# Optimization experiments

Measured on AMD Instinct MI355X. Metric: run time of the kernel, lower is better.

## Reference

```python
import jax, jax.numpy as jnp
import numpy as np

BS, L, D, H, BLOCKS = 2, 8192, 1024, 16, 16
BC = L // BLOCKS          # block_ctx = 512
HD = D // H               # head dim = 64
SCALE2 = 1.0 / float(np.sqrt(HD))  # (scale*scale) with scale = HD**-0.25


def setup_inputs() -> dict:
    key = jax.random.key(0)
    k0, k1, k2 = jax.random.split(key, 3)
    return {
        "x": jax.random.normal(k0, (BS, L, D), jnp.float32),
        "w_attn": jax.random.normal(k1, (D, 3 * D), jnp.float32) * 0.02,
        "b_attn": jnp.zeros((3 * D,), jnp.float32),
        "w_proj": jax.random.normal(k2, (D, D), jnp.float32) * 0.02,
        "b_proj": jnp.zeros((D,), jnp.float32),
    }


def _block_attn(q, k, v):
    # q, k, v: [BS, L, D]; block-local causal attention (attn_func=1, eval path)
    nb = BS * BLOCKS
    def heads(x):
        # [BS, L, D] -> [nb, BC, D] -> [nb, H, BC, HD]
        return x.reshape(nb, BC, H, HD).transpose(0, 2, 1, 3)
    qh, kh, vh = heads(q), heads(k), heads(v)
    w = jnp.einsum('bhqd,bhkd->bhqk', qh, kh) * SCALE2          # [nb, H, BC, BC]
    w = w.astype(jnp.float32)
    mask = jnp.tril(jnp.ones((BC, BC), jnp.float32))
    w = w * mask + (-1e9) * (1.0 - mask)
    w = jax.nn.softmax(w, axis=-1)
    a = jnp.einsum('bhqk,bhkd->bhqd', w, vh)                    # [nb, H, BC, HD]
    return a.transpose(0, 2, 1, 3).reshape(BS, L, D)


def reference(x, w_attn, b_attn, w_proj, b_proj):
    qkv = x @ w_attn + b_attn                                   # Conv1D c_attn
    q, k, v = jnp.split(qkv, 3, axis=-1)
    a = _block_attn(q, k, v)
    return a @ w_proj + b_proj                                  # Conv1D c_proj
```

## Files before the change

### kernel.cpp

```cpp
#include <hip/hip_runtime.h>
#include <stdint.h>


typedef __bf16 bf16x8 __attribute__((ext_vector_type(8)));
typedef short short8 __attribute__((ext_vector_type(8)));
typedef float f32x4 __attribute__((ext_vector_type(4)));
typedef unsigned short ushort4v __attribute__((ext_vector_type(4)));
typedef unsigned short ushort8v __attribute__((ext_vector_type(8)));

#define GLOAD_LDS16(g, l)                                                      \
  __builtin_amdgcn_global_load_lds(                                            \
      (const __attribute__((address_space(1))) void*)(g),                      \
      (__attribute__((address_space(3))) void*)(l), 16, 0, 0)

static __device__ __forceinline__ f32x4 mfma16(short8 a, short8 b, f32x4 c) {
  return __builtin_amdgcn_mfma_f32_16x16x32_bf16(
      __builtin_bit_cast(bf16x8, a), __builtin_bit_cast(bf16x8, b), c, 0, 0, 0);
}

static __device__ __forceinline__ unsigned short f2bf(float f) {
  unsigned u = __builtin_bit_cast(unsigned, f);
  u += 0x7FFFu + ((u >> 16) & 1u);
  return (unsigned short)(u >> 16);
}

__global__ __launch_bounds__(256) void convert_bf16(
    const float* __restrict__ in, unsigned short* __restrict__ out, int n8) {
  for (int i = blockIdx.x * 256 + threadIdx.x; i < n8; i += gridDim.x * 256) {
    f32x4 lo = *(const f32x4*)(in + (size_t)i * 8);
    f32x4 hi = *(const f32x4*)(in + (size_t)i * 8 + 4);
    ushort8v v;
    v[0] = f2bf(lo[0]); v[1] = f2bf(lo[1]); v[2] = f2bf(lo[2]); v[3] = f2bf(lo[3]);
    v[4] = f2bf(hi[0]); v[5] = f2bf(hi[1]); v[6] = f2bf(hi[2]); v[7] = f2bf(hi[3]);
    *(ushort8v*)(out + (size_t)i * 8) = v;
  }
}

__global__ __launch_bounds__(256) void transposeW(
    const float* __restrict__ in, unsigned short* __restrict__ out,
    int K, int N) {
  __shared__ float tile[64][68];
  int tn = blockIdx.x * 64, tk = blockIdx.y * 64;
  int tid = threadIdx.x;
#pragma unroll
  for (int i = 0; i < 4; ++i) {
    int ch = i * 256 + tid;
    int r = ch >> 4, c4 = (ch & 15) << 2;
    f32x4 v = *(const f32x4*)(in + (size_t)(tk + r) * N + tn + c4);
    tile[r][c4] = v[0]; tile[r][c4 + 1] = v[1];
    tile[r][c4 + 2] = v[2]; tile[r][c4 + 3] = v[3];
  }
  __syncthreads();
#pragma unroll
  for (int i = 0; i < 4; ++i) {
    int ch = i * 256 + tid;
    int r = ch >> 4, c4 = (ch & 15) << 2;
    ushort4v v;
    v[0] = f2bf(tile[c4][r]);     v[1] = f2bf(tile[c4 + 1][r]);
    v[2] = f2bf(tile[c4 + 2][r]); v[3] = f2bf(tile[c4 + 3][r]);
    *(ushort4v*)(out + (size_t)(tn + r) * K + tk + c4) = v;
  }
}

template <bool C_F32>
__global__ __launch_bounds__(512, 2) void gemm256(
    const unsigned short* __restrict__ A, int lda,
    const unsigned short* __restrict__ Bt, int ldb,
    const float* __restrict__ bias,
    void* __restrict__ Cptr, int ldc,
    int Ntiles, int K) {
  __shared__ unsigned short sA[2][256 * 64];
  __shared__ unsigned short sB[2][256 * 64];
  int bid = blockIdx.x;
  int nwg = gridDim.x;
  int swz = (bid & 7) * (nwg >> 3) + (bid >> 3);
  int bm = swz / Ntiles, bn = swz % Ntiles;
  int tid = threadIdx.x;
  int lane = tid & 63, wave = tid >> 6;
  int wr = wave >> 2, wc = wave & 3;
  int g = lane >> 4, cx = lane & 15;

  const unsigned short* srcA[4];
  const unsigned short* srcB[4];
  int dstoff[4];
#pragma unroll
  for (int i = 0; i < 4; ++i) {
    int c = i * 512 + tid;
    int r = c >> 3, pc = c & 7;
    int cc = pc ^ (r & 7);
    srcA[i] = A + (size_t)(bm * 256 + r) * lda + cc * 8;
    srcB[i] = Bt + (size_t)(bn * 256 + r) * ldb + cc * 8;
    dstoff[i] = (i * 512 + wave * 64) * 8;
  }

  f32x4 zero4 = {0.f, 0.f, 0.f, 0.f};
  f32x4 acc[8][4];
#pragma unroll
  for (int a = 0; a < 8; ++a)
#pragma unroll
    for (int b = 0; b < 4; ++b) acc[a][b] = zero4;

  int NT = K >> 6;

#pragma unroll
  for (int i = 0; i < 4; ++i) {
    GLOAD_LDS16(srcA[i], sA[0] + dstoff[i]);
    GLOAD_LDS16(srcB[i], sB[0] + dstoff[i]);
  }

  for (int t = 0; t < NT; ++t) {
    int p = t & 1;
    asm volatile("s_waitcnt vmcnt(0)" ::: "memory");
    __builtin_amdgcn_sched_barrier(0);
    __builtin_amdgcn_s_barrier();
    __builtin_amdgcn_sched_barrier(0);

    const char* bA = (const char*)sA[p];
    const char* bB = (const char*)sB[p];
    bool pre = (t + 1 < NT);
    int kt = (t + 1) * 64;
    short8 bfr[4][2];

#pragma unroll
    for (int q = 0; q < 4; ++q) {
      if (q == 0) {
#pragma unroll
        for (int ni = 0; ni < 4; ++ni)
#pragma unroll
          for (int ks = 0; ks < 2; ++ks) {
            int row = wc * 64 + ni * 16 + cx;
            unsigned off = (unsigned)(row * 128 + ks * 64 + g * 16) ^
                           ((unsigned)(row & 7) << 4);
            bfr[ni][ks] = *(const short8*)(bB + off);
          }
      }
      short8 af[2][2];
#pragma unroll
      for (int mm = 0; mm < 2; ++mm)
#pragma unroll
        for (int ks = 0; ks < 2; ++ks) {
          int row = wr * 128 + (q * 2 + mm) * 16 + cx;
          unsigned off = (unsigned)(row * 128 + ks * 64 + g * 16) ^
                         ((unsigned)(row & 7) << 4);
          af[mm][ks] = *(const short8*)(bA + off);
        }
      if (pre) {
        GLOAD_LDS16(srcA[q] + kt, sA[p ^ 1] + dstoff[q]);
        GLOAD_LDS16(srcB[q] + kt, sB[p ^ 1] + dstoff[q]);
      }
      if (q == 0) asm volatile("s_waitcnt lgkmcnt(8)" ::: "memory");
      __builtin_amdgcn_sched_barrier(0);
      __builtin_amdgcn_s_barrier();
      asm volatile("s_waitcnt lgkmcnt(0)" ::: "memory");
      __builtin_amdgcn_sched_barrier(0);
      __builtin_amdgcn_s_setprio(1);
#pragma unroll
      for (int mm = 0; mm < 2; ++mm)
#pragma unroll
        for (int ni = 0; ni < 4; ++ni)
#pragma unroll
          for (int ks = 0; ks < 2; ++ks)
            acc[q * 2 + mm][ni] = mfma16(af[mm][ks], bfr[ni][ks],
                                         acc[q * 2 + mm][ni]);
      __builtin_amdgcn_s_setprio(0);
      __builtin_amdgcn_sched_barrier(0);
      __builtin_amdgcn_s_barrier();
      __builtin_amdgcn_sched_barrier(0);
    }
  }

  float bv[4];
#pragma unroll
  for (int ni = 0; ni < 4; ++ni)
    bv[ni] = bias[bn * 256 + wc * 64 + ni * 16 + cx];

#pragma unroll
  for (int mi = 0; mi < 8; ++mi)
#pragma unroll
    for (int ni = 0; ni < 4; ++ni) {
      int col = bn * 256 + wc * 64 + ni * 16 + cx;
#pragma unroll
      for (int ri = 0; ri < 4; ++ri) {
        int row = bm * 256 + wr * 128 + mi * 16 + g * 4 + ri;
        float v = acc[mi][ni][ri] + bv[ni];
        if (C_F32)
          ((float*)Cptr)[(size_t)row * ldc + col] = v;
        else
          ((unsigned short*)Cptr)[(size_t)row * ldc + col] = f2bf(v);
      }
    }
}

__global__ __launch_bounds__(256) void attn_block(unsigned short* __restrict__ qkv) {
  const int LDQ = 3072;
  int bid = blockIdx.x;
  int pair = bid & 1;
  int nbh = bid >> 1;
  int nb = nbh >> 4, h = nbh & 15;
  int rowblk = nb << 9;
  int tid = threadIdx.x, lane = tid & 63, wave = tid >> 6;
  int g = lane >> 4, cx = lane & 15;

  __shared__ unsigned short sK[64 * 64];
  __shared__ unsigned short sVT[64 * 64];
  __shared__ unsigned short sP[4][32 * 64];
  unsigned short* myP = sP[wave];

  const unsigned short* srcK[2];
  const unsigned short* srcV[2];
  unsigned short* dstK[2];
  int kr_[2], d8_[2];
#pragma unroll
  for (int i = 0; i < 2; ++i) {
    int c = i * 256 + tid;
    int r = c >> 3, pc = c & 7, cc = pc ^ (r & 7);
    srcK[i] = qkv + (size_t)(rowblk + r) * LDQ + 1024 + h * 64 + cc * 8;
    srcV[i] = qkv + (size_t)(rowblk + r) * LDQ + 2048 + h * 64 + pc * 8;
    dstK[i] = sK + (i * 256 + wave * 64) * 8;
    kr_[i] = r; d8_[i] = pc;
  }

  f32x4 zero4 = {0.f, 0.f, 0.f, 0.f};
  const float CEXP = 0.125f * 1.44269504088896f;

  for (int qq = 0; qq < 2; ++qq) {
    int qs = qq ? (pair ? 2 : 3) : (pair ? 1 : 0);
    int ntiles = 2 * qs + 2;
    int qb0 = qs * 128 + wave * 16;

    short8 qreg[2][2];
#pragma unroll
    for (int ni = 0; ni < 2; ++ni) {
      int qrow = rowblk + qb0 + ni * 64 + cx;
      const unsigned short* qp = qkv + (size_t)qrow * LDQ + h * 64 + g * 8;
      qreg[ni][0] = *(const short8*)qp;
      qreg[ni][1] = *(const short8*)(qp + 32);
    }

    f32x4 ot[2][4];
#pragma unroll
    for (int a = 0; a < 2; ++a)
#pragma unroll
      for (int b = 0; b < 4; ++b) ot[a][b] = zero4;
    float m_run[2] = {-1e30f, -1e30f};
    float l_run[2] = {0.f, 0.f};

    for (int t = 0; t < ntiles; ++t) {
      size_t tadv = (size_t)(t * 64) * LDQ;
      short8 vv0 = *(const short8*)(srcV[0] + tadv);
      short8 vv1 = *(const short8*)(srcV[1] + tadv);
      GLOAD_LDS16(srcK[0] + tadv, dstK[0]);
      GLOAD_LDS16(srcK[1] + tadv, dstK[1]);
#pragma unroll
      for (int j = 0; j < 8; ++j) {
        int d0 = d8_[0] * 8 + j, d1 = d8_[1] * 8 + j;
        unsigned o0 = (unsigned)(d0 * 128 + kr_[0] * 2) ^
                      (unsigned)((((d8_[0] ^ j) & 7)) << 4);
        unsigned o1 = (unsigned)(d1 * 128 + kr_[1] * 2) ^
                      (unsigned)((((d8_[1] ^ j) & 7)) << 4);
        *(unsigned short*)((char*)sVT + o0) = (unsigned short)vv0[j];
        *(unsigned short*)((char*)sVT + o1) = (unsigned short)vv1[j];
      }
      __syncthreads();

      bool live0 = (t * 64) <= (qb0 + 15);

      f32x4 s[4][2];
#pragma unroll
      for (int a = 0; a < 4; ++a)
#pragma unroll
        for (int b = 0; b < 2; ++b) s[a][b] = zero4;
#pragma unroll
      for (int ks = 0; ks < 2; ++ks) {
        short8 kf[4];
#pragma unroll
        for (int mi = 0; mi < 4; ++mi) {
          int row = mi * 16 + cx;
          unsigned off = (unsigned)(row * 128 + ks * 64 + g * 16);
          off ^= (unsigned)((row & 7) << 4);
          kf[mi] = *(const short8*)((const char*)sK + off);
        }
        if (live0) {
#pragma unroll
          for (int mi = 0; mi < 4; ++mi)
            s[mi][0] = mfma16(kf[mi], qreg[0][ks], s[mi][0]);
        }
#pragma unroll
        for (int mi = 0; mi < 4; ++mi)
          s[mi][1] = mfma16(kf[mi], qreg[1][ks], s[mi][1]);
      }

      float rescv[2] = {1.f, 1.f};
#pragma unroll
      for (int ni = 0; ni < 2; ++ni) {
        if (ni == 0 && !live0) continue;
        int qbase = qb0 + ni * 64;
        int qloc = qbase + cx;
        if ((t * 64 + 63) > qbase) {
#pragma unroll
          for (int mi = 0; mi < 4; ++mi)
#pragma unroll
            for (int ri = 0; ri < 4; ++ri) {
              int kk = t * 64 + mi * 16 + g * 4 + ri;
              if (kk > qloc) s[mi][ni][ri] = -3e38f;
            }
        }
        float tm = -3e38f;
#pragma unroll
        for (int mi = 0; mi < 4; ++mi)
          tm = fmaxf(tm, fmaxf(fmaxf(s[mi][ni][0], s[mi][ni][1]),
                               fmaxf(s[mi][ni][2], s[mi][ni][3])));
        tm = fmaxf(tm, __shfl_xor(tm, 16));
        tm = fmaxf(tm, __shfl_xor(tm, 32));
        float mnew = fmaxf(m_run[ni], tm);
        float resc = exp2f((m_run[ni] - mnew) * CEXP);
        float tsum = 0.f;
#pragma unroll
        for (int mi = 0; mi < 4; ++mi)
#pragma unroll
          for (int ri = 0; ri < 4; ++ri) {
            float p = exp2f((s[mi][ni][ri] - mnew) * CEXP);
            s[mi][ni][ri] = p;
            tsum += p;
          }
        tsum += __shfl_xor(tsum, 16);
        tsum += __shfl_xor(tsum, 32);
        l_run[ni] = l_run[ni] * resc + tsum;
        m_run[ni] = mnew;
        rescv[ni] = resc;
      }

#pragma unroll
      for (int ni = 0; ni < 2; ++ni) {
        if (ni == 0 && !live0) continue;
#pragma unroll
        for (int nd = 0; nd < 4; ++nd) {
          ot[ni][nd][0] *= rescv[ni]; ot[ni][nd][1] *= rescv[ni];
          ot[ni][nd][2] *= rescv[ni]; ot[ni][nd][3] *= rescv[ni];
        }
#pragma unroll
        for (int mi = 0; mi < 4; ++mi) {
          ushort4v pk;
          pk[0] = f2bf(s[mi][ni][0]); pk[1] = f2bf(s[mi][ni][1]);
          pk[2] = f2bf(s[mi][ni][2]); pk[3] = f2bf(s[mi][ni][3]);
          int row = ni * 16 + cx;
          unsigned off = (unsigned)(row * 128 + mi * 32 + g * 8);
          off ^= (unsigned)((row & 7) << 4);
          *(ushort4v*)((char*)myP + off) = pk;
        }
      }

#pragma unroll
      for (int ks = 0; ks < 2; ++ks) {
        short8 vf[4];
#pragma unroll
        for (int nd = 0; nd < 4; ++nd) {
          int d = nd * 16 + cx;
          unsigned off = (unsigned)(d * 128 + ks * 64 + g * 16);
          off ^= (unsigned)((((d >> 3) ^ d) & 7) << 4);
          vf[nd] = *(const short8*)((const char*)sVT + off);
        }
#pragma unroll
        for (int mq = 0; mq < 2; ++mq) {
          if (mq == 0 && !live0) continue;
          int row = mq * 16 + cx;
          unsigned off = (unsigned)(row * 128 + ks * 64 + g * 16);
          off ^= (unsigned)((row & 7) << 4);
          short8 pb = *(const short8*)((const char*)myP + off);
#pragma unroll
          for (int nd = 0; nd < 4; ++nd)
            ot[mq][nd] = mfma16(vf[nd], pb, ot[mq][nd]);
        }
      }
      __syncthreads();
    }

#pragma unroll
    for (int mq = 0; mq < 2; ++mq) {
      float linv = 1.0f / fmaxf(l_run[mq], 1e-30f);
      int qrow = rowblk + qb0 + mq * 64 + cx;
#pragma unroll
      for (int nd = 0; nd < 4; ++nd) {
        ushort4v w4;
        w4[0] = f2bf(ot[mq][nd][0] * linv); w4[1] = f2bf(ot[mq][nd][1] * linv);
        w4[2] = f2bf(ot[mq][nd][2] * linv); w4[3] = f2bf(ot[mq][nd][3] * linv);
        int col = h * 64 + nd * 16 + g * 4;
        *(ushort4v*)(qkv + (size_t)qrow * LDQ + col) = w4;
      }
    }
  }
}

extern "C" void kernel_launch(void* const* d_in, const int* in_sizes, int n_in,
                              void* d_out, int out_size, void* d_ws, size_t ws_size,
                              hipStream_t stream) {
  const float* x      = (const float*)d_in[0];
  const float* w_attn = (const float*)d_in[1];
  const float* b_attn = (const float*)d_in[2];
  const float* w_proj = (const float*)d_in[3];
  const float* b_proj = (const float*)d_in[4];
  float* out = (float*)d_out;

  char* ws = (char*)d_ws;
  unsigned short* qkv = (unsigned short*)ws;
  unsigned short* wAT = (unsigned short*)(ws + (size_t)16384 * 3072 * 2);
  unsigned short* wPT = wAT + (size_t)3072 * 1024;
  unsigned short* xbf = (unsigned short*)d_out;

  transposeW<<<dim3(48, 16), 256, 0, stream>>>(w_attn, wAT, 1024, 3072);
  transposeW<<<dim3(16, 16), 256, 0, stream>>>(w_proj, wPT, 1024, 1024);
  convert_bf16<<<2048, 256, 0, stream>>>(x, xbf, 16384 * 1024 / 8);

  gemm256<false><<<768, 512, 0, stream>>>(
      xbf, 1024, wAT, 1024, b_attn, (void*)qkv, 3072, 12, 1024);

  attn_block<<<1024, 256, 0, stream>>>(qkv);

  gemm256<true><<<256, 512, 0, stream>>>(
      qkv, 3072, wPT, 1024, b_proj, (void*)out, 1024, 4, 1024);
}
```

Baseline: 245.8 us.

## Stage GEMM global-to-LDS loads with partial vmcnt waits instead of full drain

Unrolls the four K sub-phases of the bf16 GEMM main loop. It reorders the async global-to-LDS prefetch so the B tile is issued first and the A tile chunks follow in the order they are consumed. The per-iteration full `vmcnt(0)` wait before the barrier is replaced by partial `vmcnt` waits placed where each chunk is actually needed. This lets the next tile's loads overlap MFMA work instead of stalling at the start of each iteration. The correctness of the counter values depends on the exact issue order and on the row-to-chunk mapping of the LDS reads.

```diff
diff --git a/kernel.cpp b/kernel.cpp
--- a/kernel.cpp
+++ b/kernel.cpp
@@ -102,71 +102,121 @@
 
   int NT = K >> 6;
 
-#pragma unroll
-  for (int i = 0; i < 4; ++i) {
-    GLOAD_LDS16(srcA[i], sA[0] + dstoff[i]);
-    GLOAD_LDS16(srcB[i], sB[0] + dstoff[i]);
-  }
+  GLOAD_LDS16(srcB[0], sB[0] + dstoff[0]);
+  GLOAD_LDS16(srcB[1], sB[0] + dstoff[1]);
+  GLOAD_LDS16(srcB[2], sB[0] + dstoff[2]);
+  GLOAD_LDS16(srcB[3], sB[0] + dstoff[3]);
+  GLOAD_LDS16(srcA[0], sA[0] + dstoff[0]);
+  GLOAD_LDS16(srcA[2], sA[0] + dstoff[2]);
+  GLOAD_LDS16(srcA[1], sA[0] + dstoff[1]);
+  GLOAD_LDS16(srcA[3], sA[0] + dstoff[3]);
+  asm volatile("s_waitcnt vmcnt(2)" ::: "memory");
+  __builtin_amdgcn_sched_barrier(0);
+  __builtin_amdgcn_s_barrier();
+  __builtin_amdgcn_sched_barrier(0);
 
   for (int t = 0; t < NT; ++t) {
     int p = t & 1;
-    asm volatile("s_waitcnt vmcnt(0)" ::: "memory");
-    __builtin_amdgcn_sched_barrier(0);
-    __builtin_amdgcn_s_barrier();
-    __builtin_amdgcn_sched_barrier(0);
-
     const char* bA = (const char*)sA[p];
     const char* bB = (const char*)sB[p];
+    unsigned short* nA = sA[p ^ 1];
+    unsigned short* nB = sB[p ^ 1];
     bool pre = (t + 1 < NT);
     int kt = (t + 1) * 64;
     short8 bfr[4][2];
 
-#pragma unroll
-    for (int q = 0; q < 4; ++q) {
-      if (q == 0) {
-#pragma unroll
-        for (int ni = 0; ni < 4; ++ni)
-#pragma unroll
-          for (int ks = 0; ks < 2; ++ks) {
-            int row = wc * 64 + ni * 16 + cx;
-            unsigned off = (unsigned)(row * 128 + ks * 64 + g * 16) ^
-                           ((unsigned)(row & 7) << 4);
-            bfr[ni][ks] = *(const short8*)(bB + off);
-          }
-      }
-      short8 af[2][2];
-#pragma unroll
-      for (int mm = 0; mm < 2; ++mm)
+#define READ_A(afv, q)                                                         \
+  _Pragma("unroll") for (int mm = 0; mm < 2; ++mm)                             \
+      _Pragma("unroll") for (int ks = 0; ks < 2; ++ks) {                       \
+    int row = wr * 128 + ((q) * 2 + mm) * 16 + cx;                             \
+    unsigned off = (unsigned)(row * 128 + ks * 64 + g * 16) ^                  \
+                   ((unsigned)(row & 7) << 4);                                 \
+    afv[mm][ks] = *(const short8*)(bA + off);                                  \
+  }
+#define MFMA_Q(afv, q)                                                         \
+  __builtin_amdgcn_s_setprio(1);                                               \
+  _Pragma("unroll") for (int mm = 0; mm < 2; ++mm)                             \
+      _Pragma("unroll") for (int ni = 0; ni < 4; ++ni)                         \
+          _Pragma("unroll") for (int ks = 0; ks < 2; ++ks)                     \
+      acc[(q) * 2 + mm][ni] =                                                  \
+          mfma16(afv[mm][ks], bfr[ni][ks], acc[(q) * 2 + mm][ni]);             \
+  __builtin_amdgcn_s_setprio(0);
+#define PHASE_TAIL()                                                           \
+  __builtin_amdgcn_sched_barrier(0);                                           \
+  __builtin_amdgcn_s_barrier();                                                \
+  asm volatile("s_waitcnt lgkmcnt(0)" ::: "memory");                           \
+  __builtin_amdgcn_sched_barrier(0);
+#define PHASE_END()                                                            \
+  __builtin_amdgcn_sched_barrier(0);                                           \
+  __builtin_amdgcn_s_barrier();                                                \
+  __builtin_amdgcn_sched_barrier(0);
+
+    {
+#pragma unroll
+      for (int ni = 0; ni < 4; ++ni)
 #pragma unroll
         for (int ks = 0; ks < 2; ++ks) {
-          int row = wr * 128 + (q * 2 + mm) * 16 + cx;
+          int row = wc * 64 + ni * 16 + cx;
           unsigned off = (unsigned)(row * 128 + ks * 64 + g * 16) ^
                          ((unsigned)(row & 7) << 4);
-          af[mm][ks] = *(const short8*)(bA + off);
-        }
+          bfr[ni][ks] = *(const short8*)(bB + off);
+        }
+      short8 af[2][2];
+      READ_A(af, 0);
       if (pre) {
-        GLOAD_LDS16(srcA[q] + kt, sA[p ^ 1] + dstoff[q]);
-        GLOAD_LDS16(srcB[q] + kt, sB[p ^ 1] + dstoff[q]);
-      }
-      if (q == 0) asm volatile("s_waitcnt lgkmcnt(8)" ::: "memory");
+        GLOAD_LDS16(srcB[0] + kt, nB + dstoff[0]);
+        GLOAD_LDS16(srcB[1] + kt, nB + dstoff[1]);
+      }
+      asm volatile("s_waitcnt lgkmcnt(8)" ::: "memory");
+      PHASE_TAIL();
+      MFMA_Q(af, 0);
+      PHASE_END();
+    }
+    {
+      short8 af[2][2];
+      READ_A(af, 1);
+      if (pre) {
+        GLOAD_LDS16(srcB[2] + kt, nB + dstoff[2]);
+        GLOAD_LDS16(srcB[3] + kt, nB + dstoff[3]);
+      }
+      PHASE_TAIL();
+      MFMA_Q(af, 1);
       __builtin_amdgcn_sched_barrier(0);
-      __builtin_amdgcn_s_barrier();
-      asm volatile("s_waitcnt lgkmcnt(0)" ::: "memory");
+      if (pre)
+        asm volatile("s_waitcnt vmcnt(4)" ::: "memory");
+      else
+        asm volatile("s_waitcnt vmcnt(0)" ::: "memory");
+      PHASE_END();
+    }
+    {
+      short8 af[2][2];
+      READ_A(af, 2);
+      if (pre) {
+        GLOAD_LDS16(srcA[0] + kt, nA + dstoff[0]);
+        GLOAD_LDS16(srcA[2] + kt, nA + dstoff[2]);
+      }
+      PHASE_TAIL();
+      MFMA_Q(af, 2);
+      PHASE_END();
+    }
+    {
+      short8 af[2][2];
+      READ_A(af, 3);
+      if (pre) {
+        GLOAD_LDS16(srcA[1] + kt, nA + dstoff[1]);
+        GLOAD_LDS16(srcA[3] + kt, nA + dstoff[3]);
+      }
+      PHASE_TAIL();
+      MFMA_Q(af, 3);
       __builtin_amdgcn_sched_barrier(0);
-      __builtin_amdgcn_s_setprio(1);
-#pragma unroll
-      for (int mm = 0; mm < 2; ++mm)
-#pragma unroll
-        for (int ni = 0; ni < 4; ++ni)
-#pragma unroll
-          for (int ks = 0; ks < 2; ++ks)
-            acc[q * 2 + mm][ni] = mfma16(af[mm][ks], bfr[ni][ks],
-                                         acc[q * 2 + mm][ni]);
-      __builtin_amdgcn_s_setprio(0);
-      __builtin_amdgcn_sched_barrier(0);
-      __builtin_amdgcn_s_barrier();
-      __builtin_amdgcn_sched_barrier(0);
-    }
+      if (pre)
+        asm volatile("s_waitcnt vmcnt(2)" ::: "memory");
+      PHASE_END();
+    }
+#undef READ_A
+#undef MFMA_Q
+#undef PHASE_TAIL
+#undef PHASE_END
   }
 
   float bv[4];
```

Result: slower. 255.3 us (+3.8%).
